# Performance work log

Hardware: AMD Instinct MI355X
Metric: run time of the kernel (lower is better)

The kernel has to match this reference:

```python
import jax, jax.numpy as jnp
import numpy as np

N = 16384      # total nodes (8 graphs x 2048)
E = 262144     # edges (avg degree 16)
TW = 25        # time_window
H = 128        # hidden_features
POS_DIM = 2
NB = 8         # number of graphs in batch
L = 6          # hidden_layer
DT = 0.01
EPS = 1e-5
MSG_IN = 2 * H + TW + POS_DIM + 1   # 284 (actual message concat width)
UPD_IN = H + H + 1                  # 257
EMB_IN = TW + POS_DIM + 1           # 28


def _lin(key, fan_in, fan_out):
    return jax.random.normal(key, (fan_in, fan_out), jnp.float32) / np.sqrt(fan_in)


def setup_inputs() -> dict:
    key = jax.random.key(0)
    ks = jax.random.split(key, 24)
    inp = {}
    inp["u"] = jax.random.normal(ks[0], (N, TW), jnp.float32)
    inp["pos"] = jax.random.uniform(ks[1], (N, 1 + POS_DIM), jnp.float32)
    inp["edge_index"] = jax.random.randint(ks[2], (2, E), 0, N)
    inp["batch"] = jnp.sort(jax.random.randint(ks[3], (N,), 0, NB))
    # embedding MLP
    inp["emb_W1"] = _lin(ks[4], EMB_IN, H); inp["emb_b1"] = jnp.zeros((H,), jnp.float32)
    inp["emb_W2"] = _lin(ks[5], H, H);      inp["emb_b2"] = jnp.zeros((H,), jnp.float32)
    # 6 GNN layers (stacked)
    inp["msg_W1"] = jax.vmap(lambda k: _lin(k, MSG_IN, H))(jax.random.split(ks[6], L))
    inp["msg_b1"] = jnp.zeros((L, H), jnp.float32)
    inp["msg_W2"] = jax.vmap(lambda k: _lin(k, H, H))(jax.random.split(ks[7], L))
    inp["msg_b2"] = jnp.zeros((L, H), jnp.float32)
    inp["upd_W1"] = jax.vmap(lambda k: _lin(k, UPD_IN, H))(jax.random.split(ks[8], L))
    inp["upd_b1"] = jnp.zeros((L, H), jnp.float32)
    inp["upd_W2"] = jax.vmap(lambda k: _lin(k, H, H))(jax.random.split(ks[9], L))
    inp["upd_b2"] = jnp.zeros((L, H), jnp.float32)
    # output CNN: Conv1d(1,8,15,s4) -> Conv1d(8,4,10,s2) -> Conv1d(4,1,10,s1)
    inp["conv1_W"] = jax.random.normal(ks[10], (8, 1, 15), jnp.float32) / np.sqrt(15)
    inp["conv1_b"] = jnp.zeros((8,), jnp.float32)
    inp["conv2_W"] = jax.random.normal(ks[11], (4, 8, 10), jnp.float32) / np.sqrt(80)
    inp["conv2_b"] = jnp.zeros((4,), jnp.float32)
    inp["conv3_W"] = jax.random.normal(ks[12], (1, 4, 10), jnp.float32) / np.sqrt(40)
    inp["conv3_b"] = jnp.zeros((1,), jnp.float32)
    return inp


def _mlp2(x, W1, b1, W2, b2):
    return jax.nn.relu(jax.nn.relu(x @ W1 + b1) @ W2 + b2)


def _instance_norm(h, batch):
    # PyG InstanceNorm (affine=False): per-graph, per-channel normalization
    cnt = jax.ops.segment_sum(jnp.ones((h.shape[0], 1), h.dtype), batch, NB)
    cnt = jnp.maximum(cnt, 1.0)
    mean = jax.ops.segment_sum(h, batch, NB) / cnt
    meansq = jax.ops.segment_sum(h * h, batch, NB) / cnt
    var = jnp.maximum(meansq - mean * mean, 0.0)
    return (h - mean[batch]) * jax.lax.rsqrt(var[batch] + EPS)


def _gnn_layer(h, u, pos_sp, variables, src, dst, batch,
               mW1, mb1, mW2, mb2, uW1, ub1, uW2, ub2):
    # message: gather endpoints, concat, 2-layer ReLU MLP  [E, MSG_IN] -> [E, H]
    m_in = jnp.concatenate([h[dst], h[src], u[dst] - u[src],
                            pos_sp[dst] - pos_sp[src], variables[dst]], axis=-1)
    msg = _mlp2(m_in, mW1, mb1, mW2, mb2)
    # mean-scatter aggregation onto target nodes
    deg = jax.ops.segment_sum(jnp.ones((src.shape[0], 1), h.dtype), dst, N)
    agg = jax.ops.segment_sum(msg, dst, N) / jnp.maximum(deg, 1.0)
    # node update MLP + residual (in_features == out_features)
    upd = _mlp2(jnp.concatenate([h, agg, variables], axis=-1), uW1, ub1, uW2, ub2)
    return _instance_norm(h + upd, batch)


def _conv1d(x, W, b, stride):
    # x: [N, C_in, L], W: [C_out, C_in, K]
    y = jax.lax.conv_general_dilated(x, W, (stride,), 'VALID',
                                     dimension_numbers=('NCH', 'OIH', 'NCH'))
    return y + b[None, :, None]


def reference(u, pos, edge_index, batch,
              emb_W1, emb_b1, emb_W2, emb_b2,
              msg_W1, msg_b1, msg_W2, msg_b2,
              upd_W1, upd_b1, upd_W2, upd_b2,
              conv1_W, conv1_b, conv2_W, conv2_b, conv3_W, conv3_b):
    variables = pos[:, 0:1]          # time variable
    pos_sp = pos[:, 1:1 + POS_DIM]   # spatial coords
    node_input = jnp.concatenate([u, pos_sp[:, 0:1], pos_sp[:, 1:2], variables], axis=-1)
    h = _mlp2(node_input, emb_W1, emb_b1, emb_W2, emb_b2)  # [N, H]
    src, dst = edge_index[0], edge_index[1]  # PyG: row 0 = source (j), row 1 = target (i)
    for l in range(L):
        h = _gnn_layer(h, u, pos_sp, variables, src, dst, batch,
                       msg_W1[l], msg_b1[l], msg_W2[l], msg_b2[l],
                       upd_W1[l], upd_b1[l], upd_W2[l], upd_b2[l])
    # output CNN: [N,1,128] -> [N,1,1]
    y = jax.nn.relu(_conv1d(h[:, None, :], conv1_W, conv1_b, 4))
    y = jax.nn.relu(_conv1d(y, conv2_W, conv2_b, 2))
    diff = _conv1d(y, conv3_W, conv3_b, 1)[:, 0, :]        # [N, 1]
    dt = jnp.cumsum(jnp.full((1, TW), DT, jnp.float32), axis=1)
    return u[:, -1:] + dt * diff                            # [N, TW]
```

## Files before the change

kernel.cpp:

```cpp
#include <hip/hip_runtime.h>

#define NN 16384
#define NE 262144
#define TWC 25
#define HC 128
#define NBC 8
#define LC 6
#define MINC 284
#define UINC 257
#define EINC 28
#define EPSC 1e-5
#define DTC 0.01f
#define SP 65

typedef float v2f __attribute__((ext_vector_type(2)));

#define KSTEPP(ACCF, WV, ROW, KW)                                        \
  do {                                                                   \
    v2f a01_ = {sm[(ROW) * SP + e0 + 0], sm[(ROW) * SP + e0 + 1]};       \
    v2f a23_ = {sm[(ROW) * SP + e0 + 2], sm[(ROW) * SP + e0 + 3]};       \
    float4 w0_ = WV[(KW) * 32 + jg * 2];                                 \
    float4 w1_ = WV[(KW) * 32 + jg * 2 + 1];                             \
    float wv_[8] = {w0_.x, w0_.y, w0_.z, w0_.w,                          \
                    w1_.x, w1_.y, w1_.z, w1_.w};                         \
    _Pragma("unroll") for (int j_ = 0; j_ < 8; ++j_) {                   \
      v2f ws_ = {wv_[j_], wv_[j_]};                                      \
      ACCF[0][j_] = __builtin_elementwise_fma(a01_, ws_, ACCF[0][j_]);   \
      ACCF[1][j_] = __builtin_elementwise_fma(a23_, ws_, ACCF[1][j_]);   \
    }                                                                    \
  } while (0)

#define KSTEPPN(ACCF, WV, ROW, KW)                                       \
  do {                                                                   \
    v2f a01_ = {sm[(ROW) * SP + e0 + 0], sm[(ROW) * SP + e0 + 1]};       \
    v2f a23_ = {sm[(ROW) * SP + e0 + 2], sm[(ROW) * SP + e0 + 3]};       \
    a01_ = -a01_; a23_ = -a23_;                                          \
    float4 w0_ = WV[(KW) * 32 + jg * 2];                                 \
    float4 w1_ = WV[(KW) * 32 + jg * 2 + 1];                             \
    float wv_[8] = {w0_.x, w0_.y, w0_.z, w0_.w,                          \
                    w1_.x, w1_.y, w1_.z, w1_.w};                         \
    _Pragma("unroll") for (int j_ = 0; j_ < 8; ++j_) {                   \
      v2f ws_ = {wv_[j_], wv_[j_]};                                      \
      ACCF[0][j_] = __builtin_elementwise_fma(a01_, ws_, ACCF[0][j_]);   \
      ACCF[1][j_] = __builtin_elementwise_fma(a23_, ws_, ACCF[1][j_]);   \
    }                                                                    \
  } while (0)

#define FLUSH32P(ACCD, ACCF)                                             \
  do {                                                                   \
    _Pragma("unroll") for (int i_ = 0; i_ < 4; ++i_)                     \
      _Pragma("unroll") for (int j_ = 0; j_ < 8; ++j_)                   \
        ACCD[i_][j_] += (double)ACCF[i_ >> 1][j_][i_ & 1];               \
    _Pragma("unroll") for (int i_ = 0; i_ < 2; ++i_)                     \
      _Pragma("unroll") for (int j_ = 0; j_ < 8; ++j_)                   \
        ACCF[i_][j_] = (v2f){0.f, 0.f};                                  \
  } while (0)

#define ACC_INIT(ACCD, ACCF, BV)                                         \
  do {                                                                   \
    _Pragma("unroll") for (int j_ = 0; j_ < 8; ++j_) {                   \
      double bv_ = (BV);                                                 \
      _Pragma("unroll") for (int i_ = 0; i_ < 4; ++i_) ACCD[i_][j_] = bv_; \
      ACCF[0][j_] = (v2f){0.f, 0.f};                                     \
      ACCF[1][j_] = (v2f){0.f, 0.f};                                     \
    }                                                                    \
  } while (0)


__global__ __launch_bounds__(256) void k_cnt(const int* __restrict__ dst,
                                             int* __restrict__ cnt) {
  int e = blockIdx.x * 256 + threadIdx.x;
  if (e < NE) atomicAdd(&cnt[dst[e]], 1);
}

__global__ __launch_bounds__(256) void k_scan(const int* __restrict__ cnt,
                                              int* __restrict__ rowptr,
                                              int* __restrict__ fill) {
  __shared__ int part[256];
  int t = threadIdx.x;
  int s = 0;
  for (int i = 0; i < 64; ++i) s += cnt[t * 64 + i];
  part[t] = s;
  __syncthreads();
  if (t == 0) {
    int r = 0;
    for (int i = 0; i < 256; ++i) { int v = part[i]; part[i] = r; r += v; }
  }
  __syncthreads();
  int r = part[t];
  for (int i = 0; i < 64; ++i) {
    int n = t * 64 + i;
    rowptr[n] = r;
    fill[n] = r;
    r += cnt[n];
  }
  if (t == 255) rowptr[NN] = r;
}

__global__ __launch_bounds__(256) void k_scatter(const int* __restrict__ src,
                                                 const int* __restrict__ dst,
                                                 int* __restrict__ fill,
                                                 int* __restrict__ srcS,
                                                 int* __restrict__ dstS) {
  int e = blockIdx.x * 256 + threadIdx.x;
  if (e < NE) {
    int d = dst[e];
    int p = atomicAdd(&fill[d], 1);
    srcS[p] = src[e];
    dstS[p] = d;
  }
}

__global__ __launch_bounds__(256) void k_rdeg(const int* __restrict__ rowptr,
                                              float* __restrict__ rdeg) {
  int n = blockIdx.x * 256 + threadIdx.x;
  if (n < NN) {
    int c = rowptr[n + 1] - rowptr[n];
    rdeg[n] = 1.0f / (float)max(c, 1);
  }
}

__global__ __launch_bounds__(256) void k_cntb(const int* __restrict__ batch,
                                              float* __restrict__ cntb) {
  int n = blockIdx.x * 256 + threadIdx.x;
  int b = (n < NN) ? batch[n] : -1;
#pragma unroll
  for (int bb = 0; bb < NBC; ++bb) {
    unsigned long long m = __ballot(b == bb);
    if ((threadIdx.x & 63) == 0 && m != 0ULL)
      atomicAdd(&cntb[bb], (float)__popcll(m));
  }
}

__global__ __launch_bounds__(256) void k_emb(
    const float* __restrict__ u, const float* __restrict__ pos,
    const float* __restrict__ W1, const float* __restrict__ b1,
    const float* __restrict__ W2, const float* __restrict__ b2,
    float* __restrict__ h) {
  __shared__ float sin_[2][EINC];
  __shared__ float shid[2][HC];
  int n0 = blockIdx.x * 2;
  int t = threadIdx.x;
  if (t < 2 * EINC) {
    int e = t / EINC, c = t - e * EINC;
    int n = n0 + e;
    float v;
    if (c < TWC) v = u[n * TWC + c];
    else if (c == TWC) v = pos[n * 3 + 1];
    else if (c == TWC + 1) v = pos[n * 3 + 2];
    else v = pos[n * 3 + 0];
    sin_[e][c] = v;
  }
  __syncthreads();
  int e = t >> 7, j = t & 127;
  double acc = (double)b1[j];
  for (int k = 0; k < EINC; ++k)
    acc = fma((double)sin_[e][k], (double)W1[k * HC + j], acc);
  shid[e][j] = fmaxf((float)acc, 0.f);
  __syncthreads();
  double acc2 = (double)b2[j];
  for (int k = 0; k < HC; ++k)
    acc2 = fma((double)shid[e][k], (double)W2[k * HC + j], acc2);
  h[(n0 + e) * HC + j] = fmaxf((float)acc2, 0.f);
}

__global__ __launch_bounds__(256) void k_node(
    const float* __restrict__ h, const float* __restrict__ u,
    const float* __restrict__ pos, const float* __restrict__ W1,
    const float* __restrict__ b1, float* __restrict__ Dv,
    float* __restrict__ Sv) {
  __shared__ float sm[156 * SP];
  const int t = threadIdx.x;
  const int n_base = blockIdx.x * 64;
  const int isS = blockIdx.y;
  const int eg = t >> 4, jg = t & 15;
  const int e0 = eg * 4, j0 = jg * 8;
  const int half = t >> 7, col = t & 127;

  for (int it = 0; it < 32; ++it) {
    int e = 2 * it + half;
    sm[col * SP + e] = h[(n_base + e) * HC + col];
  }
  for (int idx = t; idx < 64 * 28; idx += 256) {
    int e = idx / 28, c = idx - e * 28;
    int n = n_base + e;
    float v;
    if (c < TWC) v = u[n * TWC + c];
    else if (c == TWC) v = pos[n * 3 + 1];
    else if (c == TWC + 1) v = pos[n * 3 + 2];
    else v = pos[n * 3 + 0];
    sm[(128 + c) * SP + e] = v;
  }
  __syncthreads();

  const float4* W1v = (const float4*)W1;
  v2f accf[2][8];
  double accd[4][8];
  ACC_INIT(accd, accf, isS ? 0.0 : (double)b1[j0 + j_]);

  const int wb = isS ? 128 : 0;
  for (int kc = 0; kc < 128; kc += 32) {
#pragma unroll
    for (int kk = 0; kk < 32; ++kk) KSTEPP(accf, W1v, kc + kk, wb + kc + kk);
    FLUSH32P(accd, accf);
  }
  if (!isS) {
#pragma unroll
    for (int kk = 0; kk < 28; ++kk) KSTEPP(accf, W1v, 128 + kk, 256 + kk);
  } else {
#pragma unroll
    for (int kk = 0; kk < 27; ++kk) KSTEPPN(accf, W1v, 128 + kk, 256 + kk);
  }
  FLUSH32P(accd, accf);

  float* outp = isS ? Sv : Dv;
#pragma unroll
  for (int i = 0; i < 4; ++i) {
    int n = n_base + e0 + i;
#pragma unroll
    for (int jj = 0; jj < 8; ++jj)
      outp[n * HC + j0 + jj] = (float)accd[i][jj];
  }
}

__global__ __launch_bounds__(256) void k_msg(
    const float* __restrict__ Dv, const float* __restrict__ Sv,
    const int* __restrict__ srcS, const int* __restrict__ dstS,
    const float* __restrict__ W2, const float* __restrict__ b2,
    float* __restrict__ agg) {
  __shared__ float sm[128 * SP];
  const int t = threadIdx.x;
  const int bid = blockIdx.x;
  const int e_base = ((bid & 7) * 512 + (bid >> 3)) * 64;
  const int eg = t >> 4, jg = t & 15;
  const int e0 = eg * 4, j0 = jg * 8;
  const int half = t >> 7, col = t & 127;

  if (t < 64) {
    sm[t * SP + 64] = __int_as_float(dstS[e_base + t]);
    sm[(64 + t) * SP + 64] = __int_as_float(srcS[e_base + t]);
  }
  __syncthreads();

  for (int it = 0; it < 32; ++it) {
    int e = 2 * it + half;
    int nd = __float_as_int(sm[e * SP + 64]);
    int ns = __float_as_int(sm[(64 + e) * SP + 64]);
    sm[col * SP + e] = fmaxf(Dv[nd * HC + col] + Sv[ns * HC + col], 0.f);
  }
  __syncthreads();

  v2f accf[2][8];
  double accd[4][8];
  ACC_INIT(accd, accf, (double)b2[j0 + j_]);

  const float4* W2v = (const float4*)W2;
  for (int kc = 0; kc < 128; kc += 32) {
#pragma unroll
    for (int kk = 0; kk < 32; ++kk) KSTEPP(accf, W2v, kc + kk, kc + kk);
    FLUSH32P(accd, accf);
  }
  __syncthreads();

#pragma unroll
  for (int jj = 0; jj < 8; ++jj) {
#pragma unroll
    for (int i = 0; i < 4; ++i)
      sm[(j0 + jj) * SP + e0 + i] = fmaxf((float)accd[i][jj], 0.f);
  }
  __syncthreads();

  {
    int j = t & 127;
    int ebeg = (t >> 7) * 32;
    float s = 0.f;
    int cur = __float_as_int(sm[ebeg * SP + 64]);
    for (int e = ebeg; e < ebeg + 32; ++e) {
      int d = __float_as_int(sm[e * SP + 64]);
      if (d != cur) {
        atomicAdd(&agg[cur * HC + j], s);
        s = 0.f;
        cur = d;
      }
      s += sm[j * SP + e];
    }
    atomicAdd(&agg[cur * HC + j], s);
  }
}

__global__ __launch_bounds__(256) void k_upd(
    const float* __restrict__ h, const float* __restrict__ pos,
    const float* __restrict__ agg, const float* __restrict__ rdeg,
    const int* __restrict__ batch, const float* __restrict__ W1,
    const float* __restrict__ b1, const float* __restrict__ W2,
    const float* __restrict__ b2, float* __restrict__ hn,
    double* __restrict__ stats) {
  __shared__ float sm[129 * SP];
  __shared__ int sbat[64];
  const int t = threadIdx.x;
  const int n_base = blockIdx.x * 64;
  const int eg = t >> 4, jg = t & 15;
  const int e0 = eg * 4, j0 = jg * 8;
  const int half = t >> 7, col = t & 127;

  v2f accf[2][8];
  double accd[4][8];
  ACC_INIT(accd, accf, (double)b1[j0 + j_]);

  for (int it = 0; it < 32; ++it) {
    int e = 2 * it + half;
    sm[col * SP + e] = h[(n_base + e) * HC + col];
  }
  __syncthreads();

  const float4* W1v = (const float4*)W1;
  for (int kc = 0; kc < 128; kc += 32) {
#pragma unroll
    for (int kk = 0; kk < 32; ++kk) KSTEPP(accf, W1v, kc + kk, kc + kk);
    FLUSH32P(accd, accf);
  }
  __syncthreads();

  for (int it = 0; it < 32; ++it) {
    int e = 2 * it + half;
    int n = n_base + e;
    sm[col * SP + e] = agg[n * HC + col] * rdeg[n];
  }
  if (t < 64) sm[128 * SP + t] = pos[(n_base + t) * 3 + 0];
  __syncthreads();

  for (int kc = 0; kc < 128; kc += 32) {
#pragma unroll
    for (int kk = 0; kk < 32; ++kk) KSTEPP(accf, W1v, kc + kk, 128 + kc + kk);
    FLUSH32P(accd, accf);
  }
  KSTEPP(accf, W1v, 128, 256);
  FLUSH32P(accd, accf);
  __syncthreads();

#pragma unroll
  for (int jj = 0; jj < 8; ++jj) {
#pragma unroll
    for (int i = 0; i < 4; ++i)
      sm[(j0 + jj) * SP + e0 + i] = fmaxf((float)accd[i][jj], 0.f);
  }
  __syncthreads();

  ACC_INIT(accd, accf, (double)b2[j0 + j_]);
  const float4* W2v = (const float4*)W2;
  for (int kc = 0; kc < 128; kc += 32) {
#pragma unroll
    for (int kk = 0; kk < 32; ++kk) KSTEPP(accf, W2v, kc + kk, kc + kk);
    FLUSH32P(accd, accf);
  }
  __syncthreads();

#pragma unroll
  for (int i = 0; i < 4; ++i) {
    int n = n_base + e0 + i;
#pragma unroll
    for (int jj = 0; jj < 8; ++jj) {
      int j = j0 + jj;
      float v = h[n * HC + j] + fmaxf((float)accd[i][jj], 0.f);
      hn[n * HC + j] = v;
      sm[j * SP + e0 + i] = v;
    }
  }
  if (t < 64) sbat[t] = batch[n_base + t];
  __syncthreads();

  {
    int ch = t & 127, rh = t >> 7;
    double s = 0.0, ss = 0.0;
    int cur = sbat[rh];
    for (int e = rh; e < 64; e += 2) {
      int b = sbat[e];
      double v = (double)sm[ch * SP + e];
      if (b != cur) {
        atomicAdd(&stats[cur * HC + ch], s);
        atomicAdd(&stats[NBC * HC + cur * HC + ch], ss);
        s = 0.0; ss = 0.0; cur = b;
      }
      s += v;
      ss += v * v;
    }
    atomicAdd(&stats[cur * HC + ch], s);
    atomicAdd(&stats[NBC * HC + cur * HC + ch], ss);
  }
}

__global__ __launch_bounds__(256) void k_norm(
    const float* __restrict__ hn, const int* __restrict__ batch,
    const double* __restrict__ stats, const float* __restrict__ cntb,
    float* __restrict__ hout) {
  int idx = blockIdx.x * 256 + threadIdx.x;
  int n = idx >> 7, ch = idx & 127;
  int b = batch[n];
  double c = fmax((double)cntb[b], 1.0);
  double mean = stats[b * HC + ch] / c;
  double ms = stats[NBC * HC + b * HC + ch] / c;
  double var = fmax(ms - mean * mean, 0.0);
  hout[idx] = (float)(((double)hn[idx] - mean) / sqrt(var + EPSC));
}

__global__ __launch_bounds__(64) void k_head(
    const float* __restrict__ h, const float* __restrict__ u,
    const float* __restrict__ c1W, const float* __restrict__ c1b,
    const float* __restrict__ c2W, const float* __restrict__ c2b,
    const float* __restrict__ c3W, const float* __restrict__ c3b,
    float* __restrict__ out) {
  __shared__ float hr[128];
  __shared__ float y1[8 * 29];
  __shared__ float y2[4 * 10];
  __shared__ float dv;
  int n = blockIdx.x, t = threadIdx.x;
  hr[t] = h[n * HC + t];
  hr[t + 64] = h[n * HC + 64 + t];
  __syncthreads();
  for (int idx = t; idx < 8 * 29; idx += 64) {
    int o = idx / 29, p = idx - o * 29;
    float acc = c1b[o];
    for (int q = 0; q < 15; ++q) acc = fmaf(hr[p * 4 + q], c1W[o * 15 + q], acc);
    y1[o * 29 + p] = fmaxf(acc, 0.f);
  }
  __syncthreads();
  if (t < 40) {
    int o = t / 10, p = t - o * 10;
    float acc = c2b[o];
    for (int i = 0; i < 8; ++i)
      for (int q = 0; q < 10; ++q)
        acc = fmaf(y1[i * 29 + p * 2 + q], c2W[o * 80 + i * 10 + q], acc);
    y2[o * 10 + p] = fmaxf(acc, 0.f);
  }
  __syncthreads();
  if (t == 0) {
    float acc = c3b[0];
    for (int i = 0; i < 4; ++i)
      for (int q = 0; q < 10; ++q)
        acc = fmaf(y2[i * 10 + q], c3W[i * 10 + q], acc);
    dv = acc;
  }
  __syncthreads();
  if (t < TWC) out[n * TWC + t] = u[n * TWC + 24] + DTC * (float)(t + 1) * dv;
}

extern "C" void kernel_launch(void* const* d_in, const int* in_sizes, int n_in,
                              void* d_out, int out_size, void* d_ws,
                              size_t ws_size, hipStream_t stream) {
  const float* u = (const float*)d_in[0];
  const float* pos = (const float*)d_in[1];
  const int* ei = (const int*)d_in[2];
  const int* batch = (const int*)d_in[3];
  const float* eW1 = (const float*)d_in[4];
  const float* eb1 = (const float*)d_in[5];
  const float* eW2 = (const float*)d_in[6];
  const float* eb2 = (const float*)d_in[7];
  const float* mW1 = (const float*)d_in[8];
  const float* mb1 = (const float*)d_in[9];
  const float* mW2 = (const float*)d_in[10];
  const float* mb2 = (const float*)d_in[11];
  const float* uW1 = (const float*)d_in[12];
  const float* ub1 = (const float*)d_in[13];
  const float* uW2 = (const float*)d_in[14];
  const float* ub2 = (const float*)d_in[15];
  const float* c1W = (const float*)d_in[16];
  const float* c1b = (const float*)d_in[17];
  const float* c2W = (const float*)d_in[18];
  const float* c2b = (const float*)d_in[19];
  const float* c3W = (const float*)d_in[20];
  const float* c3b = (const float*)d_in[21];
  float* out = (float*)d_out;

  const int* srcI = ei;
  const int* dstI = ei + NE;

  double* statsd = (double*)d_ws;
  float* h = (float*)(statsd + 2 * NBC * HC);
  float* Sv = h + NN * HC;
  float* agg = Sv + NN * HC;
  float* Dhn = agg + NN * HC;
  float* rdeg = Dhn + NN * HC;
  float* cntb = rdeg + NN;
  int* cnt = (int*)(cntb + NBC);
  int* rowptr = cnt + NN;
  int* fill = rowptr + NN + 1;
  int* srcS = fill + NN;
  int* dstS = srcS + NE;

  hipMemsetAsync(cnt, 0, NN * sizeof(int), stream);
  hipMemsetAsync(cntb, 0, NBC * sizeof(float), stream);
  k_cnt<<<NE / 256, 256, 0, stream>>>(dstI, cnt);
  k_scan<<<1, 256, 0, stream>>>(cnt, rowptr, fill);
  k_scatter<<<NE / 256, 256, 0, stream>>>(srcI, dstI, fill, srcS, dstS);
  k_rdeg<<<NN / 256, 256, 0, stream>>>(rowptr, rdeg);
  k_cntb<<<NN / 256, 256, 0, stream>>>(batch, cntb);
  k_emb<<<NN / 2, 256, 0, stream>>>(u, pos, eW1, eb1, eW2, eb2, h);

  for (int l = 0; l < LC; ++l) {
    hipMemsetAsync(agg, 0, (size_t)NN * HC * sizeof(float), stream);
    hipMemsetAsync(statsd, 0, 2 * NBC * HC * sizeof(double), stream);
    k_node<<<dim3(NN / 64, 2), 256, 0, stream>>>(
        h, u, pos, mW1 + (size_t)l * MINC * HC, mb1 + l * HC, Dhn, Sv);
    k_msg<<<NE / 64, 256, 0, stream>>>(Dhn, Sv, srcS, dstS,
                                       mW2 + (size_t)l * HC * HC, mb2 + l * HC,
                                       agg);
    k_upd<<<NN / 64, 256, 0, stream>>>(h, pos, agg, rdeg, batch,
                                       uW1 + (size_t)l * UINC * HC, ub1 + l * HC,
                                       uW2 + (size_t)l * HC * HC, ub2 + l * HC,
                                       Dhn, statsd);
    k_norm<<<NN * HC / 256, 256, 0, stream>>>(Dhn, batch, statsd, cntb, h);
  }
  k_head<<<NN, 64, 0, stream>>>(h, u, c1W, c1b, c2W, c2b, c3W, c3b, out);
}
```

Baseline: 2.203 ms.

## Halve node tiles in node/update kernels and fold per-layer memsets into kernels

Node and update kernels now process 32 nodes per block instead of 64 (2 rows per thread), doubling the block count to improve occupancy and CU fill. The per-layer agg memset is replaced by zeroing agg inside k_upd after it is read, and the stats memset is done by block 0 of k_node. This removes two memset launches per layer but halves per-thread register reuse of weight loads, so weights are read twice as often.

Measured after the change: 2.297 ms. 1.04x slower.

```diff
diff --git a/kernel.cpp b/kernel.cpp
--- a/kernel.cpp
+++ b/kernel.cpp
@@ -12,6 +12,7 @@
 #define EPSC 1e-5
 #define DTC 0.01f
 #define SP 65
+#define SP2 33
 
 typedef float v2f __attribute__((ext_vector_type(2)));
 
@@ -30,39 +31,69 @@
     }                                                                    \
   } while (0)
 
-#define KSTEPPN(ACCF, WV, ROW, KW)                                       \
-  do {                                                                   \
-    v2f a01_ = {sm[(ROW) * SP + e0 + 0], sm[(ROW) * SP + e0 + 1]};       \
-    v2f a23_ = {sm[(ROW) * SP + e0 + 2], sm[(ROW) * SP + e0 + 3]};       \
-    a01_ = -a01_; a23_ = -a23_;                                          \
+#define FLUSH32P(ACCD, ACCF)                                             \
+  do {                                                                   \
+    _Pragma("unroll") for (int i_ = 0; i_ < 4; ++i_)                     \
+      _Pragma("unroll") for (int j_ = 0; j_ < 8; ++j_)                   \
+        ACCD[i_][j_] += (double)ACCF[i_ >> 1][j_][i_ & 1];               \
+    _Pragma("unroll") for (int i_ = 0; i_ < 2; ++i_)                     \
+      _Pragma("unroll") for (int j_ = 0; j_ < 8; ++j_)                   \
+        ACCF[i_][j_] = (v2f){0.f, 0.f};                                  \
+  } while (0)
+
+#define ACC_INIT(ACCD, ACCF, BV)                                         \
+  do {                                                                   \
+    _Pragma("unroll") for (int j_ = 0; j_ < 8; ++j_) {                   \
+      double bv_ = (BV);                                                 \
+      _Pragma("unroll") for (int i_ = 0; i_ < 4; ++i_) ACCD[i_][j_] = bv_; \
+      ACCF[0][j_] = (v2f){0.f, 0.f};                                     \
+      ACCF[1][j_] = (v2f){0.f, 0.f};                                     \
+    }                                                                    \
+  } while (0)
+
+#define KSTEPQ(ACCF, WV, ROW, KW)                                        \
+  do {                                                                   \
+    v2f a_ = {sm[(ROW) * SP2 + e0], sm[(ROW) * SP2 + e0 + 1]};           \
     float4 w0_ = WV[(KW) * 32 + jg * 2];                                 \
     float4 w1_ = WV[(KW) * 32 + jg * 2 + 1];                             \
     float wv_[8] = {w0_.x, w0_.y, w0_.z, w0_.w,                          \
                     w1_.x, w1_.y, w1_.z, w1_.w};                         \
     _Pragma("unroll") for (int j_ = 0; j_ < 8; ++j_) {                   \
       v2f ws_ = {wv_[j_], wv_[j_]};                                      \
-      ACCF[0][j_] = __builtin_elementwise_fma(a01_, ws_, ACCF[0][j_]);   \
-      ACCF[1][j_] = __builtin_elementwise_fma(a23_, ws_, ACCF[1][j_]);   \
+      ACCF[j_] = __builtin_elementwise_fma(a_, ws_, ACCF[j_]);           \
     }                                                                    \
   } while (0)
 
-#define FLUSH32P(ACCD, ACCF)                                             \
-  do {                                                                   \
-    _Pragma("unroll") for (int i_ = 0; i_ < 4; ++i_)                     \
-      _Pragma("unroll") for (int j_ = 0; j_ < 8; ++j_)                   \
-        ACCD[i_][j_] += (double)ACCF[i_ >> 1][j_][i_ & 1];               \
-    _Pragma("unroll") for (int i_ = 0; i_ < 2; ++i_)                     \
-      _Pragma("unroll") for (int j_ = 0; j_ < 8; ++j_)                   \
-        ACCF[i_][j_] = (v2f){0.f, 0.f};                                  \
-  } while (0)
-
-#define ACC_INIT(ACCD, ACCF, BV)                                         \
+#define KSTEPQN(ACCF, WV, ROW, KW)                                       \
+  do {                                                                   \
+    v2f a_ = {sm[(ROW) * SP2 + e0], sm[(ROW) * SP2 + e0 + 1]};           \
+    a_ = -a_;                                                            \
+    float4 w0_ = WV[(KW) * 32 + jg * 2];                                 \
+    float4 w1_ = WV[(KW) * 32 + jg * 2 + 1];                             \
+    float wv_[8] = {w0_.x, w0_.y, w0_.z, w0_.w,                          \
+                    w1_.x, w1_.y, w1_.z, w1_.w};                         \
+    _Pragma("unroll") for (int j_ = 0; j_ < 8; ++j_) {                   \
+      v2f ws_ = {wv_[j_], wv_[j_]};                                      \
+      ACCF[j_] = __builtin_elementwise_fma(a_, ws_, ACCF[j_]);           \
+    }                                                                    \
+  } while (0)
+
+#define FLUSHQ(ACCD, ACCF)                                               \
+  do {                                                                   \
+    _Pragma("unroll") for (int j_ = 0; j_ < 8; ++j_) {                   \
+      ACCD[0][j_] += (double)ACCF[j_][0];                                \
+      ACCD[1][j_] += (double)ACCF[j_][1];                                \
+      ACCF[j_] = (v2f){0.f, 0.f};                                        \
+    }                                                                    \
+  } while (0)
+
+#define ACC_INITQ(ACCD, ACCF, BV)                                        \
   do {                                                                   \
     _Pragma("unroll") for (int j_ = 0; j_ < 8; ++j_) {                   \
       double bv_ = (BV);                                                 \
-      _Pragma("unroll") for (int i_ = 0; i_ < 4; ++i_) ACCD[i_][j_] = bv_; \
-      ACCF[0][j_] = (v2f){0.f, 0.f};                                     \
-      ACCF[1][j_] = (v2f){0.f, 0.f};                                     \
+      ACCD[0][j_] = bv_;                                                 \
+      ACCD[1][j_] = bv_;                                                 \
+      ACCF[j_] = (v2f){0.f, 0.f};                                        \
     }                                                                    \
   } while (0)
 
@@ -168,20 +199,24 @@
     const float* __restrict__ h, const float* __restrict__ u,
     const float* __restrict__ pos, const float* __restrict__ W1,
     const float* __restrict__ b1, float* __restrict__ Dv,
-    float* __restrict__ Sv) {
-  __shared__ float sm[156 * SP];
+    float* __restrict__ Sv, double* __restrict__ stats) {
+  __shared__ float sm[156 * SP2];
   const int t = threadIdx.x;
-  const int n_base = blockIdx.x * 64;
+  const int n_base = blockIdx.x * 32;
   const int isS = blockIdx.y;
   const int eg = t >> 4, jg = t & 15;
-  const int e0 = eg * 4, j0 = jg * 8;
+  const int e0 = eg * 2, j0 = jg * 8;
   const int half = t >> 7, col = t & 127;
 
-  for (int it = 0; it < 32; ++it) {
+  if (blockIdx.x == 0 && isS == 0) {
+    for (int i = t; i < 2 * NBC * HC; i += 256) stats[i] = 0.0;
+  }
+
+  for (int it = 0; it < 16; ++it) {
     int e = 2 * it + half;
-    sm[col * SP + e] = h[(n_base + e) * HC + col];
-  }
-  for (int idx = t; idx < 64 * 28; idx += 256) {
+    sm[col * SP2 + e] = h[(n_base + e) * HC + col];
+  }
+  for (int idx = t; idx < 32 * 28; idx += 256) {
     int e = idx / 28, c = idx - e * 28;
     int n = n_base + e;
     float v;
@@ -189,33 +224,33 @@
     else if (c == TWC) v = pos[n * 3 + 1];
     else if (c == TWC + 1) v = pos[n * 3 + 2];
     else v = pos[n * 3 + 0];
-    sm[(128 + c) * SP + e] = v;
+    sm[(128 + c) * SP2 + e] = v;
   }
   __syncthreads();
 
   const float4* W1v = (const float4*)W1;
-  v2f accf[2][8];
-  double accd[4][8];
-  ACC_INIT(accd, accf, isS ? 0.0 : (double)b1[j0 + j_]);
+  v2f accf[8];
+  double accd[2][8];
+  ACC_INITQ(accd, accf, isS ? 0.0 : (double)b1[j0 + j_]);
 
   const int wb = isS ? 128 : 0;
   for (int kc = 0; kc < 128; kc += 32) {
 #pragma unroll
-    for (int kk = 0; kk < 32; ++kk) KSTEPP(accf, W1v, kc + kk, wb + kc + kk);
-    FLUSH32P(accd, accf);
+    for (int kk = 0; kk < 32; ++kk) KSTEPQ(accf, W1v, kc + kk, wb + kc + kk);
+    FLUSHQ(accd, accf);
   }
   if (!isS) {
 #pragma unroll
-    for (int kk = 0; kk < 28; ++kk) KSTEPP(accf, W1v, 128 + kk, 256 + kk);
+    for (int kk = 0; kk < 28; ++kk) KSTEPQ(accf, W1v, 128 + kk, 256 + kk);
   } else {
 #pragma unroll
-    for (int kk = 0; kk < 27; ++kk) KSTEPPN(accf, W1v, 128 + kk, 256 + kk);
-  }
-  FLUSH32P(accd, accf);
+    for (int kk = 0; kk < 27; ++kk) KSTEPQN(accf, W1v, 128 + kk, 256 + kk);
+  }
+  FLUSHQ(accd, accf);
 
   float* outp = isS ? Sv : Dv;
 #pragma unroll
-  for (int i = 0; i < 4; ++i) {
+  for (int i = 0; i < 2; ++i) {
     int n = n_base + e0 + i;
 #pragma unroll
     for (int jj = 0; jj < 8; ++jj)
@@ -290,92 +325,93 @@
 
 __global__ __launch_bounds__(256) void k_upd(
     const float* __restrict__ h, const float* __restrict__ pos,
-    const float* __restrict__ agg, const float* __restrict__ rdeg,
+    float* __restrict__ agg, const float* __restrict__ rdeg,
     const int* __restrict__ batch, const float* __restrict__ W1,
     const float* __restrict__ b1, const float* __restrict__ W2,
     const float* __restrict__ b2, float* __restrict__ hn,
     double* __restrict__ stats) {
-  __shared__ float sm[129 * SP];
-  __shared__ int sbat[64];
+  __shared__ float sm[129 * SP2];
+  __shared__ int sbat[32];
   const int t = threadIdx.x;
-  const int n_base = blockIdx.x * 64;
+  const int n_base = blockIdx.x * 32;
   const int eg = t >> 4, jg = t & 15;
-  const int e0 = eg * 4, j0 = jg * 8;
+  const int e0 = eg * 2, j0 = jg * 8;
   const int half = t >> 7, col = t & 127;
 
-  v2f accf[2][8];
-  double accd[4][8];
-  ACC_INIT(accd, accf, (double)b1[j0 + j_]);
-
-  for (int it = 0; it < 32; ++it) {
+  v2f accf[8];
+  double accd[2][8];
+  ACC_INITQ(accd, accf, (double)b1[j0 + j_]);
+
+  for (int it = 0; it < 16; ++it) {
     int e = 2 * it + half;
-    sm[col * SP + e] = h[(n_base + e) * HC + col];
+    sm[col * SP2 + e] = h[(n_base + e) * HC + col];
   }
   __syncthreads();
 
   const float4* W1v = (const float4*)W1;
   for (int kc = 0; kc < 128; kc += 32) {
 #pragma unroll
-    for (int kk = 0; kk < 32; ++kk) KSTEPP(accf, W1v, kc + kk, kc + kk);
-    FLUSH32P(accd, accf);
-  }
-  __syncthreads();
-
-  for (int it = 0; it < 32; ++it) {
+    for (int kk = 0; kk < 32; ++kk) KSTEPQ(accf, W1v, kc + kk, kc + kk);
+    FLUSHQ(accd, accf);
+  }
+  __syncthreads();
+
+  for (int it = 0; it < 16; ++it) {
     int e = 2 * it + half;
     int n = n_base + e;
-    sm[col * SP + e] = agg[n * HC + col] * rdeg[n];
-  }
-  if (t < 64) sm[128 * SP + t] = pos[(n_base + t) * 3 + 0];
+    sm[col * SP2 + e] = agg[n * HC + col] * rdeg[n];
+    agg[n * HC + col] = 0.f;
+  }
+  if (t < 32) sm[128 * SP2 + t] = pos[(n_base + t) * 3 + 0];
   __syncthreads();
 
   for (int kc = 0; kc < 128; kc += 32) {
 #pragma unroll
-    for (int kk = 0; kk < 32; ++kk) KSTEPP(accf, W1v, kc + kk, 128 + kc + kk);
-    FLUSH32P(accd, accf);
-  }
-  KSTEPP(accf, W1v, 128, 256);
-  FLUSH32P(accd, accf);
+    for (int kk = 0; kk < 32; ++kk) KSTEPQ(accf, W1v, kc + kk, 128 + kc + kk);
+    FLUSHQ(accd, accf);
+  }
+  KSTEPQ(accf, W1v, 128, 256);
+  FLUSHQ(accd, accf);
   __syncthreads();
 
 #pragma unroll
   for (int jj = 0; jj < 8; ++jj) {
 #pragma unroll
-    for (int i = 0; i < 4; ++i)
-      sm[(j0 + jj) * SP + e0 + i] = fmaxf((float)accd[i][jj], 0.f);
-  }
-  __syncthreads();
-
-  ACC_INIT(accd, accf, (double)b2[j0 + j_]);
+    for (int i = 0; i < 2; ++i)
+      sm[(j0 + jj) * SP2 + e0 + i] = fmaxf((float)accd[i][jj], 0.f);
+  }
+  __syncthreads();
+
+  ACC_INITQ(accd, accf, (double)b2[j0 + j_]);
   const float4* W2v = (const float4*)W2;
   for (int kc = 0; kc < 128; kc += 32) {
 #pragma unroll
-    for (int kk = 0; kk < 32; ++kk) KSTEPP(accf, W2v, kc + kk, kc + kk);
-    FLUSH32P(accd, accf);
-  }
-  __syncthreads();
-
-#pragma unroll
-  for (int i = 0; i < 4; ++i) {
+    for (int kk = 0; kk < 32; ++kk) KSTEPQ(accf, W2v, kc + kk, kc + kk);
+    FLUSHQ(accd, accf);
+  }
+  __syncthreads();
+
+#pragma unroll
+  for (int i = 0; i < 2; ++i) {
     int n = n_base + e0 + i;
 #pragma unroll
     for (int jj = 0; jj < 8; ++jj) {
       int j = j0 + jj;
       float v = h[n * HC + j] + fmaxf((float)accd[i][jj], 0.f);
       hn[n * HC + j] = v;
-      sm[j * SP + e0 + i] = v;
+      sm[j * SP2 + e0 + i] = v;
     }
   }
-  if (t < 64) sbat[t] = batch[n_base + t];
+  if (t < 32) sbat[t] = batch[n_base + t];
   __syncthreads();
 
   {
     int ch = t & 127, rh = t >> 7;
     double s = 0.0, ss = 0.0;
     int cur = sbat[rh];
-    for (int e = rh; e < 64; e += 2) {
+    for (int e = rh; e < 32; e += 2) {
       int b = sbat[e];
-      double v = (double)sm[ch * SP + e];
+      double v = (double)sm[ch * SP2 + e];
       if (b != cur) {
         atomicAdd(&stats[cur * HC + ch], s);
         atomicAdd(&stats[NBC * HC + cur * HC + ch], ss);
@@ -489,6 +525,7 @@
 
   hipMemsetAsync(cnt, 0, NN * sizeof(int), stream);
   hipMemsetAsync(cntb, 0, NBC * sizeof(float), stream);
+  hipMemsetAsync(agg, 0, (size_t)NN * HC * sizeof(float), stream);
   k_cnt<<<NE / 256, 256, 0, stream>>>(dstI, cnt);
   k_scan<<<1, 256, 0, stream>>>(cnt, rowptr, fill);
   k_scatter<<<NE / 256, 256, 0, stream>>>(srcI, dstI, fill, srcS, dstS);
@@ -497,14 +534,12 @@
   k_emb<<<NN / 2, 256, 0, stream>>>(u, pos, eW1, eb1, eW2, eb2, h);
 
   for (int l = 0; l < LC; ++l) {
-    hipMemsetAsync(agg, 0, (size_t)NN * HC * sizeof(float), stream);
-    hipMemsetAsync(statsd, 0, 2 * NBC * HC * sizeof(double), stream);
-    k_node<<<dim3(NN / 64, 2), 256, 0, stream>>>(
-        h, u, pos, mW1 + (size_t)l * MINC * HC, mb1 + l * HC, Dhn, Sv);
+    k_node<<<dim3(NN / 32, 2), 256, 0, stream>>>(
+        h, u, pos, mW1 + (size_t)l * MINC * HC, mb1 + l * HC, Dhn, Sv, statsd);
     k_msg<<<NE / 64, 256, 0, stream>>>(Dhn, Sv, srcS, dstS,
                                        mW2 + (size_t)l * HC * HC, mb2 + l * HC,
                                        agg);
-    k_upd<<<NN / 64, 256, 0, stream>>>(h, pos, agg, rdeg, batch,
+    k_upd<<<NN / 32, 256, 0, stream>>>(h, pos, agg, rdeg, batch,
                                        uW1 + (size_t)l * UINC * HC, ub1 + l * HC,
                                        uW2 + (size_t)l * HC * HC, ub2 + l * HC,
                                        Dhn, statsd);
```

## Vectorize msg gather, overlap second-half gather with GEMM, fold memsets into kernels

Applied to the files above, without the earlier changes.

k_msg now gathers edge features with float4 loads and keeps edge indices in their own shared arrays. It loads the second half of the feature columns into registers while the first half of the K loop runs, hiding gather latency behind compute. The per-layer memsets of agg and stats are removed: k_upd zeroes agg after reading it, and k_node block 0 zeroes the stats. This saves two memset launches and a full write pass per layer, at the cost of extra register pressure in k_msg. It also relies on k_upd reading all of agg before it is reused.

New measurement: 2.586 ms. +17.4%, slower.

```diff
diff --git a/kernel.cpp b/kernel.cpp
--- a/kernel.cpp
+++ b/kernel.cpp
@@ -168,7 +168,7 @@
     const float* __restrict__ h, const float* __restrict__ u,
     const float* __restrict__ pos, const float* __restrict__ W1,
     const float* __restrict__ b1, float* __restrict__ Dv,
-    float* __restrict__ Sv) {
+    float* __restrict__ Sv, double* __restrict__ stats) {
   __shared__ float sm[156 * SP];
   const int t = threadIdx.x;
   const int n_base = blockIdx.x * 64;
@@ -176,6 +176,10 @@
   const int eg = t >> 4, jg = t & 15;
   const int e0 = eg * 4, j0 = jg * 8;
   const int half = t >> 7, col = t & 127;
+
+  if (blockIdx.x == 0 && isS == 0) {
+    for (int i = t; i < 2 * NBC * HC; i += 256) stats[i] = 0.0;
+  }
 
   for (int it = 0; it < 32; ++it) {
     int e = 2 * it + half;
@@ -229,33 +233,65 @@
     const float* __restrict__ W2, const float* __restrict__ b2,
     float* __restrict__ agg) {
   __shared__ float sm[128 * SP];
+  __shared__ int sdst[64];
+  __shared__ int ssrc[64];
   const int t = threadIdx.x;
   const int bid = blockIdx.x;
   const int e_base = ((bid & 7) * 512 + (bid >> 3)) * 64;
   const int eg = t >> 4, jg = t & 15;
   const int e0 = eg * 4, j0 = jg * 8;
-  const int half = t >> 7, col = t & 127;
+  const int q = t & 15, el = t >> 4;
 
   if (t < 64) {
-    sm[t * SP + 64] = __int_as_float(dstS[e_base + t]);
-    sm[(64 + t) * SP + 64] = __int_as_float(srcS[e_base + t]);
-  }
-  __syncthreads();
-
-  for (int it = 0; it < 32; ++it) {
-    int e = 2 * it + half;
-    int nd = __float_as_int(sm[e * SP + 64]);
-    int ns = __float_as_int(sm[(64 + e) * SP + 64]);
-    sm[col * SP + e] = fmaxf(Dv[nd * HC + col] + Sv[ns * HC + col], 0.f);
-  }
-  __syncthreads();
+    sdst[t] = dstS[e_base + t];
+    ssrc[t] = srcS[e_base + t];
+  }
+  __syncthreads();
+
+#pragma unroll
+  for (int it = 0; it < 4; ++it) {
+    int e = it * 16 + el;
+    int nd = sdst[e], ns = ssrc[e];
+    float4 d4 = *(const float4*)&Dv[nd * HC + q * 4];
+    float4 s4 = *(const float4*)&Sv[ns * HC + q * 4];
+    sm[(q * 4 + 0) * SP + e] = fmaxf(d4.x + s4.x, 0.f);
+    sm[(q * 4 + 1) * SP + e] = fmaxf(d4.y + s4.y, 0.f);
+    sm[(q * 4 + 2) * SP + e] = fmaxf(d4.z + s4.z, 0.f);
+    sm[(q * 4 + 3) * SP + e] = fmaxf(d4.w + s4.w, 0.f);
+  }
+  __syncthreads();
+
+  float4 bd[4], bs[4];
+#pragma unroll
+  for (int it = 0; it < 4; ++it) {
+    int e = it * 16 + el;
+    int nd = sdst[e], ns = ssrc[e];
+    bd[it] = *(const float4*)&Dv[nd * HC + 64 + q * 4];
+    bs[it] = *(const float4*)&Sv[ns * HC + 64 + q * 4];
+  }
 
   v2f accf[2][8];
   double accd[4][8];
   ACC_INIT(accd, accf, (double)b2[j0 + j_]);
-
   const float4* W2v = (const float4*)W2;
-  for (int kc = 0; kc < 128; kc += 32) {
+
+  for (int kc = 0; kc < 64; kc += 32) {
+#pragma unroll
+    for (int kk = 0; kk < 32; ++kk) KSTEPP(accf, W2v, kc + kk, kc + kk);
+    FLUSH32P(accd, accf);
+  }
+
+#pragma unroll
+  for (int it = 0; it < 4; ++it) {
+    int e = it * 16 + el;
+    sm[(64 + q * 4 + 0) * SP + e] = fmaxf(bd[it].x + bs[it].x, 0.f);
+    sm[(64 + q * 4 + 1) * SP + e] = fmaxf(bd[it].y + bs[it].y, 0.f);
+    sm[(64 + q * 4 + 2) * SP + e] = fmaxf(bd[it].z + bs[it].z, 0.f);
+    sm[(64 + q * 4 + 3) * SP + e] = fmaxf(bd[it].w + bs[it].w, 0.f);
+  }
+  __syncthreads();
+
+  for (int kc = 64; kc < 128; kc += 32) {
 #pragma unroll
     for (int kk = 0; kk < 32; ++kk) KSTEPP(accf, W2v, kc + kk, kc + kk);
     FLUSH32P(accd, accf);
@@ -274,9 +310,9 @@
     int j = t & 127;
     int ebeg = (t >> 7) * 32;
     float s = 0.f;
-    int cur = __float_as_int(sm[ebeg * SP + 64]);
+    int cur = sdst[ebeg];
     for (int e = ebeg; e < ebeg + 32; ++e) {
-      int d = __float_as_int(sm[e * SP + 64]);
+      int d = sdst[e];
       if (d != cur) {
         atomicAdd(&agg[cur * HC + j], s);
         s = 0.f;
@@ -290,7 +326,7 @@
 
 __global__ __launch_bounds__(256) void k_upd(
     const float* __restrict__ h, const float* __restrict__ pos,
-    const float* __restrict__ agg, const float* __restrict__ rdeg,
+    float* __restrict__ agg, const float* __restrict__ rdeg,
     const int* __restrict__ batch, const float* __restrict__ W1,
     const float* __restrict__ b1, const float* __restrict__ W2,
     const float* __restrict__ b2, float* __restrict__ hn,
@@ -325,6 +361,7 @@
     int e = 2 * it + half;
     int n = n_base + e;
     sm[col * SP + e] = agg[n * HC + col] * rdeg[n];
+    agg[n * HC + col] = 0.f;
   }
   if (t < 64) sm[128 * SP + t] = pos[(n_base + t) * 3 + 0];
   __syncthreads();
@@ -489,6 +526,7 @@
 
   hipMemsetAsync(cnt, 0, NN * sizeof(int), stream);
   hipMemsetAsync(cntb, 0, NBC * sizeof(float), stream);
+  hipMemsetAsync(agg, 0, (size_t)NN * HC * sizeof(float), stream);
   k_cnt<<<NE / 256, 256, 0, stream>>>(dstI, cnt);
   k_scan<<<1, 256, 0, stream>>>(cnt, rowptr, fill);
   k_scatter<<<NE / 256, 256, 0, stream>>>(srcI, dstI, fill, srcS, dstS);
@@ -497,10 +535,8 @@
   k_emb<<<NN / 2, 256, 0, stream>>>(u, pos, eW1, eb1, eW2, eb2, h);
 
   for (int l = 0; l < LC; ++l) {
-    hipMemsetAsync(agg, 0, (size_t)NN * HC * sizeof(float), stream);
-    hipMemsetAsync(statsd, 0, 2 * NBC * HC * sizeof(double), stream);
     k_node<<<dim3(NN / 64, 2), 256, 0, stream>>>(
-        h, u, pos, mW1 + (size_t)l * MINC * HC, mb1 + l * HC, Dhn, Sv);
+        h, u, pos, mW1 + (size_t)l * MINC * HC, mb1 + l * HC, Dhn, Sv, statsd);
     k_msg<<<NE / 64, 256, 0, stream>>>(Dhn, Sv, srcS, dstS,
                                        mW2 + (size_t)l * HC * HC, mb2 + l * HC,
                                        agg);
```
